# Optimization experiments

Measured on AMD Instinct MI355X. Metric: run time of the kernel, lower is better.

Reference implementation:

```python
import jax, jax.numpy as jnp
import numpy as np

N_USERS = 500_000
N_ITEMS = 200_000
D_FEAT = 256
H = 32
N_EDGES = 2_000_000
NEG_SLOPE = 0.01


def _lin(k, out_dim, in_dim):
    return jax.random.normal(k, (out_dim, in_dim), jnp.float32) * (1.0 / np.sqrt(in_dim))


def setup_inputs() -> dict:
    key = jax.random.key(0)
    ks = jax.random.split(key, 24)
    src = jax.random.randint(ks[0], (N_EDGES,), 0, N_USERS)   # user ids
    dst = jax.random.randint(ks[1], (N_EDGES,), 0, N_ITEMS)   # product ids
    inp = {
        "user_ids": jnp.arange(N_USERS, dtype=jnp.int32),
        "product_ids": jnp.arange(N_ITEMS, dtype=jnp.int32),
        "product_features": jax.random.normal(ks[2], (N_ITEMS, D_FEAT), jnp.float32),
        "edge_rates": jnp.stack([src, dst]),      # user -> product
        "edge_rated_by": jnp.stack([dst, src]),   # product -> user (reverse)
        "user_emb": jax.random.normal(ks[3], (N_USERS, H), jnp.float32),
        "item_emb": jax.random.normal(ks[4], (N_ITEMS, H), jnp.float32),
        "feat_W": _lin(ks[5], H, D_FEAT),
        "feat_b": jnp.zeros((H,), jnp.float32),
    }
    # SAGEConv params: lin_l (neighbor, with bias), lin_r (root, no bias)
    names = ["up1", "pu1", "up2", "pu2"]  # up = user->product conv, pu = product->user conv
    for i, n in enumerate(names):
        inp[f"Wl_{n}"] = _lin(ks[6 + 3 * i], H, H)
        inp[f"bl_{n}"] = jnp.zeros((H,), jnp.float32)
        inp[f"Wr_{n}"] = _lin(ks[7 + 3 * i], H, H)
    return inp


def _sage(x_src, x_dst, edge_index, Wl, bl, Wr):
    # PyG SAGEConv, aggr='mean': lin_l(mean_j x_src[j]) + lin_r(x_dst)
    e_src, e_dst = edge_index[0], edge_index[1]
    n_dst = x_dst.shape[0]
    msg_sum = jax.ops.segment_sum(x_src[e_src], e_dst, num_segments=n_dst)
    cnt = jax.ops.segment_sum(jnp.ones_like(e_dst, dtype=x_src.dtype), e_dst, num_segments=n_dst)
    mean = msg_sum / jnp.maximum(cnt, 1.0)[:, None]
    return mean @ Wl.T + bl + x_dst @ Wr.T


def reference(user_ids, product_ids, product_features, edge_rates, edge_rated_by,
              user_emb, item_emb, feat_W, feat_b,
              Wl_up1, bl_up1, Wr_up1, Wl_pu1, bl_pu1, Wr_pu1,
              Wl_up2, bl_up2, Wr_up2, Wl_pu2, bl_pu2, Wr_pu2):
    lrelu = lambda x: jax.nn.leaky_relu(x, NEG_SLOPE)
    xu = user_emb[user_ids]                                    # [Nu, H]
    xp = item_emb[product_ids] + product_features @ feat_W.T + feat_b  # [Ni, H]

    # layer 1 (HeteroConv: each node type has exactly one incoming relation)
    p1 = lrelu(_sage(xu, xp, edge_rates, Wl_up1, bl_up1, Wr_up1))
    u1 = lrelu(_sage(xp, xu, edge_rated_by, Wl_pu1, bl_pu1, Wr_pu1))
    # layer 2
    p2 = lrelu(_sage(u1, p1, edge_rates, Wl_up2, bl_up2, Wr_up2))
    u2 = lrelu(_sage(p1, u1, edge_rated_by, Wl_pu2, bl_pu2, Wr_pu2))

    final_user = jnp.concatenate([xu, u1, u2], axis=1)   # [Nu, 3H]
    final_item = jnp.concatenate([xp, p1, p2], axis=1)   # [Ni, 3H]
    return final_user, final_item
```

## Files before the change

kernel.cpp:

```cpp
#include <hip/hip_runtime.h>

#define NU 500000
#define NI 200000
#define NE 2000000
#define HD 32
#define DF 256
#define OC 96

__device__ __forceinline__ float lrelu(float v){ return v >= 0.f ? v : 0.01f*v; }

__global__ void k_zero_i32(int* __restrict__ p, int n){
  int i = blockIdx.x*blockDim.x + threadIdx.x;
  if (i < n) p[i] = 0;
}

__global__ void k_init_user(const int* __restrict__ ids, const float* __restrict__ emb,
                            float* __restrict__ outu){
  int i = blockIdx.x*blockDim.x + threadIdx.x;
  if (i >= NU) return;
  int uid = ids[i];
  const float4* s = (const float4*)(emb + (size_t)uid*HD);
  float4* d = (float4*)(outu + (size_t)i*OC);
  #pragma unroll
  for (int q = 0; q < 8; ++q) d[q] = s[q];
  float4 z = make_float4(0.f,0.f,0.f,0.f);
  #pragma unroll
  for (int q = 8; q < 24; ++q) d[q] = z;
}

__global__ void k_init_item(const int* __restrict__ ids, const float* __restrict__ emb,
                            const float* __restrict__ feat, const float* __restrict__ W,
                            const float* __restrict__ b, float* __restrict__ outi){
  int i = blockIdx.x*blockDim.x + threadIdx.x;
  if (i >= NI) return;
  int pid = ids[i];
  float acc[HD];
  const float4* ev = (const float4*)(emb + (size_t)pid*HD);
  #pragma unroll
  for (int q = 0; q < 8; ++q) {
    float4 e4 = ev[q];
    acc[q*4+0] = e4.x + b[q*4+0];
    acc[q*4+1] = e4.y + b[q*4+1];
    acc[q*4+2] = e4.z + b[q*4+2];
    acc[q*4+3] = e4.w + b[q*4+3];
  }
  const float* f = feat + (size_t)i*DF;
  for (int k0 = 0; k0 < DF; k0 += 8) {
    float4 a0 = *(const float4*)(f + k0);
    float4 a1 = *(const float4*)(f + k0 + 4);
    float fv[8] = {a0.x,a0.y,a0.z,a0.w,a1.x,a1.y,a1.z,a1.w};
    #pragma unroll
    for (int kk = 0; kk < 8; ++kk) {
      #pragma unroll
      for (int h = 0; h < HD; ++h) acc[h] += fv[kk]*W[h*DF + k0 + kk];
    }
  }
  float* dst = outi + (size_t)i*OC;
  #pragma unroll
  for (int q = 0; q < 8; ++q)
    ((float4*)dst)[q] = make_float4(acc[q*4+0], acc[q*4+1], acc[q*4+2], acc[q*4+3]);
  float4 z = make_float4(0.f,0.f,0.f,0.f);
  #pragma unroll
  for (int q = 8; q < 24; ++q) ((float4*)dst)[q] = z;
}

__global__ void k_deg(const int* __restrict__ esrc, const int* __restrict__ edst,
                      int* __restrict__ cnt_u, int* __restrict__ cnt_p){
  int e = blockIdx.x*blockDim.x + threadIdx.x;
  if (e >= NE) return;
  atomicAdd(cnt_u + esrc[e], 1);
  atomicAdd(cnt_p + edst[e], 1);
}

__global__ void k_agg(const float* __restrict__ srcbase, int soff,
                      const int* __restrict__ esrc, const int* __restrict__ edst,
                      float* __restrict__ accbase, int aoff){
  int t = blockIdx.x*blockDim.x + threadIdx.x;
  int e = t >> 5;
  if (e >= NE) return;
  int h = t & 31;
  int s = esrc[e], d = edst[e];
  atomicAdd(accbase + (size_t)d*OC + aoff + h, srcbase[(size_t)s*OC + soff + h]);
}

__global__ void k_fin(float* __restrict__ base, int n, int accoff, int xoff, int outoff,
                      const int* __restrict__ cnt, const float* __restrict__ Wl,
                      const float* __restrict__ bl, const float* __restrict__ Wr){
  int i = blockIdx.x*blockDim.x + threadIdx.x;
  if (i >= n) return;
  float* row = base + (size_t)i*OC;
  int c = cnt[i]; if (c < 1) c = 1;
  float inv = 1.f/(float)c;
  float m[HD], x[HD];
  #pragma unroll
  for (int q = 0; q < 8; ++q) {
    float4 a = *(const float4*)(row + accoff + q*4);
    m[q*4+0]=a.x*inv; m[q*4+1]=a.y*inv; m[q*4+2]=a.z*inv; m[q*4+3]=a.w*inv;
    float4 xx = *(const float4*)(row + xoff + q*4);
    x[q*4+0]=xx.x; x[q*4+1]=xx.y; x[q*4+2]=xx.z; x[q*4+3]=xx.w;
  }
  float y[HD];
  #pragma unroll
  for (int h = 0; h < HD; ++h) {
    float s = bl[h];
    #pragma unroll
    for (int j = 0; j < HD; ++j) s += m[j]*Wl[h*HD+j];
    #pragma unroll
    for (int j = 0; j < HD; ++j) s += x[j]*Wr[h*HD+j];
    y[h] = lrelu(s);
  }
  #pragma unroll
  for (int q = 0; q < 8; ++q)
    *((float4*)(row + outoff + q*4)) = make_float4(y[q*4+0],y[q*4+1],y[q*4+2],y[q*4+3]);
}

extern "C" void kernel_launch(void* const* d_in, const int* in_sizes, int n_in,
                              void* d_out, int out_size, void* d_ws, size_t ws_size,
                              hipStream_t stream) {
  const int*   user_ids = (const int*)d_in[0];
  const int*   prod_ids = (const int*)d_in[1];
  const float* feat     = (const float*)d_in[2];
  const int*   er       = (const int*)d_in[3];
  const int*   erb      = (const int*)d_in[4];
  const float* uemb     = (const float*)d_in[5];
  const float* iemb     = (const float*)d_in[6];
  const float* fW       = (const float*)d_in[7];
  const float* fb       = (const float*)d_in[8];
  const float* Wl_up1 = (const float*)d_in[9];
  const float* bl_up1 = (const float*)d_in[10];
  const float* Wr_up1 = (const float*)d_in[11];
  const float* Wl_pu1 = (const float*)d_in[12];
  const float* bl_pu1 = (const float*)d_in[13];
  const float* Wr_pu1 = (const float*)d_in[14];
  const float* Wl_up2 = (const float*)d_in[15];
  const float* bl_up2 = (const float*)d_in[16];
  const float* Wr_up2 = (const float*)d_in[17];
  const float* Wl_pu2 = (const float*)d_in[18];
  const float* bl_pu2 = (const float*)d_in[19];
  const float* Wr_pu2 = (const float*)d_in[20];

  float* outu = (float*)d_out;
  float* outi = outu + (size_t)NU*OC;
  int* cnt_u = (int*)d_ws;
  int* cnt_p = cnt_u + NU;

  const int* er_src  = er;
  const int* er_dst  = er + NE;
  const int* erb_src = erb;
  const int* erb_dst = erb + NE;

  const int B = 256;
  k_zero_i32<<<(NU+NI+B-1)/B, B, 0, stream>>>(cnt_u, NU+NI);
  k_init_user<<<(NU+B-1)/B, B, 0, stream>>>(user_ids, uemb, outu);
  k_init_item<<<(NI+B-1)/B, B, 0, stream>>>(prod_ids, iemb, feat, fW, fb, outi);
  k_deg<<<(NE+B-1)/B, B, 0, stream>>>(er_src, er_dst, cnt_u, cnt_p);

  const int agrid = (NE*32 + B - 1)/B;
  k_agg<<<agrid, B, 0, stream>>>(outu, 0, er_src, er_dst, outi, 32);
  k_agg<<<agrid, B, 0, stream>>>(outi, 0, erb_src, erb_dst, outu, 32);
  k_fin<<<(NI+B-1)/B, B, 0, stream>>>(outi, NI, 32, 0, 32, cnt_p, Wl_up1, bl_up1, Wr_up1);
  k_fin<<<(NU+B-1)/B, B, 0, stream>>>(outu, NU, 32, 0, 32, cnt_u, Wl_pu1, bl_pu1, Wr_pu1);
  k_agg<<<agrid, B, 0, stream>>>(outu, 32, er_src, er_dst, outi, 64);
  k_agg<<<agrid, B, 0, stream>>>(outi, 32, erb_src, erb_dst, outu, 64);
  k_fin<<<(NI+B-1)/B, B, 0, stream>>>(outi, NI, 64, 32, 64, cnt_p, Wl_up2, bl_up2, Wr_up2);
  k_fin<<<(NU+B-1)/B, B, 0, stream>>>(outu, NU, 64, 32, 64, cnt_u, Wl_pu2, bl_pu2, Wr_pu2);
}
```

Measured before the change: 1.623 ms.

## Rewrite pipeline with bf16 gather tables, packed bf16 atomics, and MFMA feature projection

Replaces most of the pipeline. Node features become compact bf16 tables that are gathered per edge, and scatter uses packed bf16 atomic adds into separate compact accumulators. The item feature projection now runs on MFMA bf16 instructions, and edge_rated_by is dropped in favour of swapped edge_rates index arrays. This cuts gather/atomic bytes and the scalar GEMM cost, but accumulating sums in bf16 atomics and feeding bf16 inputs to the dense layers may exceed the accuracy tolerance.

Result: slower. 1.943 ms (+19.7%).

```diff
diff --git a/kernel.cpp b/kernel.cpp
--- a/kernel.cpp
+++ b/kernel.cpp
@@ -2,102 +2,152 @@
 
 #define NU 500000
 #define NI 200000
+#define NN (NU + NI)
 #define NE 2000000
 #define HD 32
 #define DF 256
 #define OC 96
 
+typedef float        f4  __attribute__((ext_vector_type(4)));
+typedef unsigned int u2  __attribute__((ext_vector_type(2)));
+typedef unsigned int u4v __attribute__((ext_vector_type(4)));
+typedef short        s8v __attribute__((ext_vector_type(8)));
+typedef unsigned short ushort_t;
+
 __device__ __forceinline__ float lrelu(float v){ return v >= 0.f ? v : 0.01f*v; }
 
-__global__ void k_zero_i32(int* __restrict__ p, int n){
-  int i = blockIdx.x*blockDim.x + threadIdx.x;
-  if (i < n) p[i] = 0;
-}
-
-__global__ void k_init_user(const int* __restrict__ ids, const float* __restrict__ emb,
-                            float* __restrict__ outu){
-  int i = blockIdx.x*blockDim.x + threadIdx.x;
-  if (i >= NU) return;
-  int uid = ids[i];
-  const float4* s = (const float4*)(emb + (size_t)uid*HD);
-  float4* d = (float4*)(outu + (size_t)i*OC);
-  #pragma unroll
-  for (int q = 0; q < 8; ++q) d[q] = s[q];
-  float4 z = make_float4(0.f,0.f,0.f,0.f);
-  #pragma unroll
-  for (int q = 8; q < 24; ++q) d[q] = z;
-}
-
-__global__ void k_init_item(const int* __restrict__ ids, const float* __restrict__ emb,
-                            const float* __restrict__ feat, const float* __restrict__ W,
-                            const float* __restrict__ b, float* __restrict__ outi){
-  int i = blockIdx.x*blockDim.x + threadIdx.x;
-  if (i >= NI) return;
-  int pid = ids[i];
-  float acc[HD];
-  const float4* ev = (const float4*)(emb + (size_t)pid*HD);
-  #pragma unroll
-  for (int q = 0; q < 8; ++q) {
-    float4 e4 = ev[q];
-    acc[q*4+0] = e4.x + b[q*4+0];
-    acc[q*4+1] = e4.y + b[q*4+1];
-    acc[q*4+2] = e4.z + b[q*4+2];
-    acc[q*4+3] = e4.w + b[q*4+3];
-  }
-  const float* f = feat + (size_t)i*DF;
-  for (int k0 = 0; k0 < DF; k0 += 8) {
-    float4 a0 = *(const float4*)(f + k0);
-    float4 a1 = *(const float4*)(f + k0 + 4);
-    float fv[8] = {a0.x,a0.y,a0.z,a0.w,a1.x,a1.y,a1.z,a1.w};
-    #pragma unroll
-    for (int kk = 0; kk < 8; ++kk) {
-      #pragma unroll
-      for (int h = 0; h < HD; ++h) acc[h] += fv[kk]*W[h*DF + k0 + kk];
-    }
-  }
-  float* dst = outi + (size_t)i*OC;
-  #pragma unroll
-  for (int q = 0; q < 8; ++q)
-    ((float4*)dst)[q] = make_float4(acc[q*4+0], acc[q*4+1], acc[q*4+2], acc[q*4+3]);
-  float4 z = make_float4(0.f,0.f,0.f,0.f);
-  #pragma unroll
-  for (int q = 8; q < 24; ++q) ((float4*)dst)[q] = z;
+__device__ __forceinline__ unsigned int f2bf(float f){
+  unsigned int u = __float_as_uint(f);
+  u += 0x7fffu + ((u >> 16) & 1u);
+  return u >> 16;
+}
+__device__ __forceinline__ float bflo(unsigned int u){ return __uint_as_float(u << 16); }
+__device__ __forceinline__ float bfhi(unsigned int u){ return __uint_as_float(u & 0xffff0000u); }
+
+__device__ __forceinline__ s8v pack8(f4 a, f4 b){
+  s8v r;
+  r[0]=(short)f2bf(a.x); r[1]=(short)f2bf(a.y); r[2]=(short)f2bf(a.z); r[3]=(short)f2bf(a.w);
+  r[4]=(short)f2bf(b.x); r[5]=(short)f2bf(b.y); r[6]=(short)f2bf(b.z); r[7]=(short)f2bf(b.w);
+  return r;
 }
 
 __global__ void k_deg(const int* __restrict__ esrc, const int* __restrict__ edst,
-                      int* __restrict__ cnt_u, int* __restrict__ cnt_p){
+                      int* __restrict__ cnt){
   int e = blockIdx.x*blockDim.x + threadIdx.x;
   if (e >= NE) return;
-  atomicAdd(cnt_u + esrc[e], 1);
-  atomicAdd(cnt_p + edst[e], 1);
-}
-
-__global__ void k_agg(const float* __restrict__ srcbase, int soff,
-                      const int* __restrict__ esrc, const int* __restrict__ edst,
-                      float* __restrict__ accbase, int aoff){
-  int t = blockIdx.x*blockDim.x + threadIdx.x;
-  int e = t >> 5;
+  int u = __builtin_nontemporal_load(esrc + e);
+  int p = __builtin_nontemporal_load(edst + e);
+  atomicAdd(cnt + u, 1);
+  atomicAdd(cnt + NU + p, 1);
+}
+
+__global__ void k_init_user(const int* __restrict__ ids, const float* __restrict__ emb,
+                            float* __restrict__ outu, ushort_t* __restrict__ tbl){
+  int tid = blockIdx.x*256 + threadIdx.x;
+  int node = tid >> 3;
+  if (node >= NU) return;
+  int q = tid & 7;
+  int uid = ids[node];
+  f4 v = *((const f4*)(emb + (size_t)uid*HD) + q);
+  __builtin_nontemporal_store(v, (f4*)(outu + (size_t)node*OC) + q);
+  u2 pv; pv.x = f2bf(v.x) | (f2bf(v.y) << 16); pv.y = f2bf(v.z) | (f2bf(v.w) << 16);
+  ((u2*)tbl)[(size_t)node*8 + q] = pv;
+}
+
+__global__ __launch_bounds__(256) void k_init_item_mfma(
+    const int* __restrict__ ids, const float* __restrict__ emb,
+    const float* __restrict__ feat, const float* __restrict__ W,
+    const float* __restrict__ bias, float* __restrict__ outi){
+  int wave = threadIdx.x >> 6;
+  int lane = threadIdx.x & 63;
+  int tile = blockIdx.x*4 + wave;
+  int row0 = tile*16;
+  if (row0 >= NI) return;
+  int m = lane & 15, grp = lane >> 4;
+
+  s8v bfrag[16];
+  #pragma unroll
+  for (int ks = 0; ks < 8; ++ks) {
+    #pragma unroll
+    for (int nh = 0; nh < 2; ++nh) {
+      const float* wp = W + (size_t)(nh*16 + m)*DF + ks*32 + grp*8;
+      f4 w0 = *(const f4*)wp;
+      f4 w1 = *(const f4*)(wp + 4);
+      bfrag[ks*2 + nh] = pack8(w0, w1);
+    }
+  }
+
+  f4 acc0 = {0,0,0,0}, acc1 = {0,0,0,0};
+  const float* fr = feat + (size_t)(row0 + m)*DF + grp*8;
+  #pragma unroll
+  for (int ks = 0; ks < 8; ++ks) {
+    f4 a0 = *(const f4*)(fr + ks*32);
+    f4 a1 = *(const f4*)(fr + ks*32 + 4);
+    s8v af = pack8(a0, a1);
+    acc0 = __builtin_amdgcn_mfma_f32_16x16x32_bf16(af, bfrag[ks*2+0], acc0, 0, 0, 0);
+    acc1 = __builtin_amdgcn_mfma_f32_16x16x32_bf16(af, bfrag[ks*2+1], acc1, 0, 0, 0);
+  }
+
+  #pragma unroll
+  for (int j = 0; j < 4; ++j) {
+    int r = row0 + grp*4 + j;
+    int pid = ids[r];
+    float v0 = acc0[j] + emb[(size_t)pid*HD + m]      + bias[m];
+    float v1 = acc1[j] + emb[(size_t)pid*HD + 16 + m] + bias[16 + m];
+    outi[(size_t)r*OC + m]      = v0;
+    outi[(size_t)r*OC + 16 + m] = v1;
+  }
+}
+
+__global__ void k_tbl_item(const float* __restrict__ outi, ushort_t* __restrict__ tbl){
+  int tid = blockIdx.x*256 + threadIdx.x;
+  int node = tid >> 3;
+  if (node >= NI) return;
+  int q = tid & 7;
+  f4 v = *((const f4*)(outi + (size_t)node*OC) + q);
+  u2 pv; pv.x = f2bf(v.x) | (f2bf(v.y) << 16); pv.y = f2bf(v.z) | (f2bf(v.w) << 16);
+  ((u2*)tbl)[(size_t)node*8 + q] = pv;
+}
+
+__global__ void k_push(const ushort_t* __restrict__ tbl,
+                       const int* __restrict__ eS, const int* __restrict__ eD,
+                       ushort_t* __restrict__ acc){
+  int tid = blockIdx.x*256 + threadIdx.x;
+  int e = tid >> 3;
   if (e >= NE) return;
-  int h = t & 31;
-  int s = esrc[e], d = edst[e];
-  atomicAdd(accbase + (size_t)d*OC + aoff + h, srcbase[(size_t)s*OC + soff + h]);
-}
-
-__global__ void k_fin(float* __restrict__ base, int n, int accoff, int xoff, int outoff,
-                      const int* __restrict__ cnt, const float* __restrict__ Wl,
-                      const float* __restrict__ bl, const float* __restrict__ Wr){
+  int q = tid & 7;
+  int s = __builtin_nontemporal_load(eS + e);
+  int d = __builtin_nontemporal_load(eD + e);
+  u2 v = ((const u2*)tbl)[(size_t)s*8 + q];
+  ushort_t* a = acc + (size_t)d*HD + q*4;
+  asm volatile("global_atomic_pk_add_bf16 %0, %1, off"          :: "v"(a), "v"(v.x) : "memory");
+  asm volatile("global_atomic_pk_add_bf16 %0, %1, off offset:4" :: "v"(a), "v"(v.y) : "memory");
+}
+
+__global__ void k_fin3(float* __restrict__ dstbase, int n,
+                       const ushort_t* __restrict__ acc, const int* __restrict__ cnt,
+                       const ushort_t* __restrict__ xtbl, int outoff,
+                       const float* __restrict__ Wl, const float* __restrict__ bl,
+                       const float* __restrict__ Wr, ushort_t* __restrict__ tblout){
   int i = blockIdx.x*blockDim.x + threadIdx.x;
   if (i >= n) return;
-  float* row = base + (size_t)i*OC;
-  int c = cnt[i]; if (c < 1) c = 1;
-  float inv = 1.f/(float)c;
+  int c = cnt[i];
+  float inv = (c > 0) ? 1.f/(float)c : 0.f;
   float m[HD], x[HD];
-  #pragma unroll
-  for (int q = 0; q < 8; ++q) {
-    float4 a = *(const float4*)(row + accoff + q*4);
-    m[q*4+0]=a.x*inv; m[q*4+1]=a.y*inv; m[q*4+2]=a.z*inv; m[q*4+3]=a.w*inv;
-    float4 xx = *(const float4*)(row + xoff + q*4);
-    x[q*4+0]=xx.x; x[q*4+1]=xx.y; x[q*4+2]=xx.z; x[q*4+3]=xx.w;
+  const u4v* ar = (const u4v*)(acc + (size_t)i*HD);
+  const u4v* xr = (const u4v*)(xtbl + (size_t)i*HD);
+  #pragma unroll
+  for (int t = 0; t < 4; ++t) {
+    u4v v = ar[t];
+    m[8*t+0] = bflo(v.x)*inv; m[8*t+1] = bfhi(v.x)*inv;
+    m[8*t+2] = bflo(v.y)*inv; m[8*t+3] = bfhi(v.y)*inv;
+    m[8*t+4] = bflo(v.z)*inv; m[8*t+5] = bfhi(v.z)*inv;
+    m[8*t+6] = bflo(v.w)*inv; m[8*t+7] = bfhi(v.w)*inv;
+    u4v xv = xr[t];
+    x[8*t+0] = bflo(xv.x); x[8*t+1] = bfhi(xv.x);
+    x[8*t+2] = bflo(xv.y); x[8*t+3] = bfhi(xv.y);
+    x[8*t+4] = bflo(xv.z); x[8*t+5] = bfhi(xv.z);
+    x[8*t+6] = bflo(xv.w); x[8*t+7] = bfhi(xv.w);
   }
   float y[HD];
   #pragma unroll
@@ -109,9 +159,25 @@
     for (int j = 0; j < HD; ++j) s += x[j]*Wr[h*HD+j];
     y[h] = lrelu(s);
   }
-  #pragma unroll
-  for (int q = 0; q < 8; ++q)
-    *((float4*)(row + outoff + q*4)) = make_float4(y[q*4+0],y[q*4+1],y[q*4+2],y[q*4+3]);
+  float* row = dstbase + (size_t)i*OC + outoff;
+  #pragma unroll
+  for (int qq = 0; qq < 8; ++qq) {
+    f4 yo; yo.x=y[4*qq+0]; yo.y=y[4*qq+1]; yo.z=y[4*qq+2]; yo.w=y[4*qq+3];
+    __builtin_nontemporal_store(yo, (f4*)row + qq);
+  }
+  if (tblout) {
+    u4v pv[4];
+    #pragma unroll
+    for (int t = 0; t < 4; ++t) {
+      pv[t].x = f2bf(y[8*t+0]) | (f2bf(y[8*t+1]) << 16);
+      pv[t].y = f2bf(y[8*t+2]) | (f2bf(y[8*t+3]) << 16);
+      pv[t].z = f2bf(y[8*t+4]) | (f2bf(y[8*t+5]) << 16);
+      pv[t].w = f2bf(y[8*t+6]) | (f2bf(y[8*t+7]) << 16);
+    }
+    u4v* tb = (u4v*)(tblout + (size_t)i*HD);
+    #pragma unroll
+    for (int t = 0; t < 4; ++t) tb[t] = pv[t];
+  }
 }
 
 extern "C" void kernel_launch(void* const* d_in, const int* in_sizes, int n_in,
@@ -121,7 +187,6 @@
   const int*   prod_ids = (const int*)d_in[1];
   const float* feat     = (const float*)d_in[2];
   const int*   er       = (const int*)d_in[3];
-  const int*   erb      = (const int*)d_in[4];
   const float* uemb     = (const float*)d_in[5];
   const float* iemb     = (const float*)d_in[6];
   const float* fW       = (const float*)d_in[7];
@@ -141,27 +206,47 @@
 
   float* outu = (float*)d_out;
   float* outi = outu + (size_t)NU*OC;
-  int* cnt_u = (int*)d_ws;
-  int* cnt_p = cnt_u + NU;
-
-  const int* er_src  = er;
-  const int* er_dst  = er + NE;
-  const int* erb_src = erb;
-  const int* erb_dst = erb + NE;
+
+  char* w = (char*)d_ws;
+  int* cnt = (int*)w;                         w += ((size_t)NN*4 + 255) & ~(size_t)255;
+  ushort_t* tblU  = (ushort_t*)w;             w += (size_t)NU*HD*2;
+  ushort_t* tblI  = (ushort_t*)w;             w += (size_t)NI*HD*2;
+  ushort_t* tblU2 = (ushort_t*)w;             w += (size_t)NU*HD*2;
+  ushort_t* tblI2 = (ushort_t*)w;             w += (size_t)NI*HD*2;
+  ushort_t* accU  = (ushort_t*)w;             w += (size_t)NU*HD*2;
+  ushort_t* accI  = (ushort_t*)w;
+
+  const int* er_src = er;
+  const int* er_dst = er + NE;
 
   const int B = 256;
-  k_zero_i32<<<(NU+NI+B-1)/B, B, 0, stream>>>(cnt_u, NU+NI);
-  k_init_user<<<(NU+B-1)/B, B, 0, stream>>>(user_ids, uemb, outu);
-  k_init_item<<<(NI+B-1)/B, B, 0, stream>>>(prod_ids, iemb, feat, fW, fb, outi);
-  k_deg<<<(NE+B-1)/B, B, 0, stream>>>(er_src, er_dst, cnt_u, cnt_p);
-
-  const int agrid = (NE*32 + B - 1)/B;
-  k_agg<<<agrid, B, 0, stream>>>(outu, 0, er_src, er_dst, outi, 32);
-  k_agg<<<agrid, B, 0, stream>>>(outi, 0, erb_src, erb_dst, outu, 32);
-  k_fin<<<(NI+B-1)/B, B, 0, stream>>>(outi, NI, 32, 0, 32, cnt_p, Wl_up1, bl_up1, Wr_up1);
-  k_fin<<<(NU+B-1)/B, B, 0, stream>>>(outu, NU, 32, 0, 32, cnt_u, Wl_pu1, bl_pu1, Wr_pu1);
-  k_agg<<<agrid, B, 0, stream>>>(outu, 32, er_src, er_dst, outi, 64);
-  k_agg<<<agrid, B, 0, stream>>>(outi, 32, erb_src, erb_dst, outu, 64);
-  k_fin<<<(NI+B-1)/B, B, 0, stream>>>(outi, NI, 64, 32, 64, cnt_p, Wl_up2, bl_up2, Wr_up2);
-  k_fin<<<(NU+B-1)/B, B, 0, stream>>>(outu, NU, 64, 32, 64, cnt_u, Wl_pu2, bl_pu2, Wr_pu2);
-}
+  const int GE  = (NE + B - 1)/B;
+  const int GE8 = ((size_t)NE*8 + B - 1)/B;
+  const int GU8 = ((size_t)NU*8 + B - 1)/B, GI8 = ((size_t)NI*8 + B - 1)/B;
+  const int GU1 = (NU + B - 1)/B,           GI1 = (NI + B - 1)/B;
+  const size_t accU_bytes = (size_t)NU*HD*2, accI_bytes = (size_t)NI*HD*2;
+
+  hipMemsetAsync(cnt, 0, (size_t)NN*4, stream);
+  k_deg<<<GE, B, 0, stream>>>(er_src, er_dst, cnt);
+
+  k_init_user<<<GU8, B, 0, stream>>>(user_ids, uemb, outu, tblU);
+  k_init_item_mfma<<<(NI + 63)/64, 256, 0, stream>>>(prod_ids, iemb, feat, fW, fb, outi);
+  k_tbl_item<<<GI8, B, 0, stream>>>(outi, tblI);
+
+  hipMemsetAsync(accI, 0, accI_bytes, stream);
+  k_push<<<GE8, B, 0, stream>>>(tblU, er_src, er_dst, accI);
+  k_fin3<<<GI1, B, 0, stream>>>(outi, NI, accI, cnt + NU, tblI, 32,
+                                Wl_up1, bl_up1, Wr_up1, tblI2);
+  hipMemsetAsync(accU, 0, accU_bytes, stream);
+  k_push<<<GE8, B, 0, stream>>>(tblI, er_dst, er_src, accU);
+  k_fin3<<<GU1, B, 0, stream>>>(outu, NU, accU, cnt, tblU, 32,
+                                Wl_pu1, bl_pu1, Wr_pu1, tblU2);
+  hipMemsetAsync(accI, 0, accI_bytes, stream);
+  k_push<<<GE8, B, 0, stream>>>(tblU2, er_src, er_dst, accI);
+  k_fin3<<<GI1, B, 0, stream>>>(outi, NI, accI, cnt + NU, tblI2, 64,
+                                Wl_up2, bl_up2, Wr_up2, (ushort_t*)nullptr);
+  hipMemsetAsync(accU, 0, accU_bytes, stream);
+  k_push<<<GE8, B, 0, stream>>>(tblI2, er_dst, er_src, accU);
+  k_fin3<<<GU1, B, 0, stream>>>(outu, NU, accU, cnt, tblU2, 64,
+                                Wl_pu2, bl_pu2, Wr_pu2, (ushort_t*)nullptr);
+}
```
